# Kernel optimization log

Hardware: AMD Instinct MI355X
Metric: run time of the kernel (lower is better)

## Reference

```python
import jax, jax.numpy as jnp
import numpy as np

GROUPS = 32
EPS = 1e-5
NUM_HEADS = 8

def group_norm(x, w, b):
    # x: [B, C, H, W], normalize over (C//G, H, W) per group
    B, C, H, W = x.shape
    xg = x.reshape(B, GROUPS, C // GROUPS, H, W)
    mean = xg.mean(axis=(2, 3, 4), keepdims=True)
    var = xg.var(axis=(2, 3, 4), keepdims=True)
    xg = (xg - mean) * jax.lax.rsqrt(var + EPS)
    x = xg.reshape(B, C, H, W)
    return x * w[None, :, None, None] + b[None, :, None, None]

def setup_inputs() -> dict:
    key = jax.random.key(0)
    ks = jax.random.split(key, 3)
    C = 512
    x = jax.random.normal(ks[0], (8, C, 32, 32), dtype=jnp.float32)
    gn_w = jnp.ones((C,), jnp.float32)
    gn_b = jnp.zeros((C,), jnp.float32)
    # 1x1 conv weights stored as [out, in] matrices
    qkv_w = jax.random.normal(ks[1], (3 * C, C), dtype=jnp.float32) * (C ** -0.5)
    qkv_b = jnp.zeros((3 * C,), jnp.float32)
    proj_w = jax.random.normal(ks[2], (C, C), dtype=jnp.float32) * (C ** -0.5)
    proj_b = jnp.zeros((C,), jnp.float32)
    return {"x": x, "gn_w": gn_w, "gn_b": gn_b, "qkv_w": qkv_w,
            "qkv_b": qkv_b, "proj_w": proj_w, "proj_b": proj_b}

def reference(x, gn_w, gn_b, qkv_w, qkv_b, proj_w, proj_b):
    B, C, H, W = x.shape
    nh = NUM_HEADS
    hd = C // nh
    N = H * W
    residual = x
    xn = group_norm(x, gn_w, gn_b)
    # 1x1 conv == channel matmul: [B, 3C, H, W]
    qkv = jnp.einsum('bchw,oc->bohw', xn, qkv_w) + qkv_b[None, :, None, None]
    # [B, 3, nh, hd, N] -> q/k/v each [B, nh, N, hd]
    qkv = qkv.reshape(B, 3, nh, hd, N).transpose(1, 0, 2, 4, 3)
    q, k, v = qkv[0], qkv[1], qkv[2]
    scale = hd ** -0.5
    attn = jnp.einsum('bhqd,bhkd->bhqk', q, k) * scale
    attn = jax.nn.softmax(attn, axis=-1)
    out = jnp.einsum('bhqk,bhkd->bhqd', attn, v)  # [B, nh, N, hd]
    out = out.transpose(0, 1, 3, 2).reshape(B, C, H, W)
    out = jnp.einsum('bchw,oc->bohw', out, proj_w) + proj_b[None, :, None, None]
    return out + residual
```

## Files before the change

### kernel.cpp

```cpp
#include <hip/hip_runtime.h>


typedef __bf16 bf16;
typedef __bf16 bf16x8 __attribute__((ext_vector_type(8)));
typedef __bf16 bf16x4 __attribute__((ext_vector_type(4)));
typedef float  f32x4  __attribute__((ext_vector_type(4)));

#define MFMA_16x16x32(A, B, C) __builtin_amdgcn_mfma_f32_16x16x32_bf16((A), (B), (C), 0, 0, 0)

static __device__ __forceinline__ void async_stage_128x32(
    const bf16* __restrict__ g0, bf16* lds, int tid) {
  const int wv = tid >> 6, ln = tid & 63;
#pragma unroll
  for (int cc = 0; cc < 2; ++cc) {
    const int c = wv + cc * 4;
    const bf16* g = g0 + (size_t)(c * 16 + (ln >> 2)) * 512 + (ln & 3) * 8;
    __builtin_amdgcn_global_load_lds(
        (const __attribute__((address_space(1))) void*)g,
        (__attribute__((address_space(3))) void*)(lds + c * 512),
        16, 0, 0);
  }
}

__global__ void wconv_kernel(const float* __restrict__ qw, const float* __restrict__ pw,
                             bf16* __restrict__ wq, bf16* __restrict__ wp) {
  const int i = blockIdx.x * 256 + threadIdx.x;
  if (i < 1536 * 512) wq[i] = (bf16)qw[i];
  if (i < 512 * 512)  wp[i] = (bf16)pw[i];
}

__global__ void gn_stats_kernel(const float* __restrict__ x,
                                float* __restrict__ meanp, float* __restrict__ rstdp) {
  const int bg = blockIdx.x;
  const float4* p = (const float4*)(x + (size_t)bg * 16384);
  float s = 0.f, s2 = 0.f;
#pragma unroll 4
  for (int i = threadIdx.x; i < 4096; i += 256) {
    float4 v = p[i];
    s  += (v.x + v.y) + (v.z + v.w);
    s2 += (v.x * v.x + v.y * v.y) + (v.z * v.z + v.w * v.w);
  }
#pragma unroll
  for (int d = 1; d < 64; d <<= 1) {
    s  += __shfl_xor(s,  d);
    s2 += __shfl_xor(s2, d);
  }
  __shared__ float as[4], as2[4];
  if ((threadIdx.x & 63) == 0) { as[threadIdx.x >> 6] = s; as2[threadIdx.x >> 6] = s2; }
  __syncthreads();
  if (threadIdx.x == 0) {
    float S  = as[0] + as[1] + as[2] + as[3];
    float S2 = as2[0] + as2[1] + as2[2] + as2[3];
    float m = S * (1.0f / 16384.0f);
    float v = S2 * (1.0f / 16384.0f) - m * m;
    meanp[bg] = m;
    rstdp[bg] = rsqrtf(v + 1e-5f);
  }
}

__global__ void gn_apply_kernel(const float* __restrict__ x,
                                const float* __restrict__ gn_w, const float* __restrict__ gn_b,
                                const float* __restrict__ meanp, const float* __restrict__ rstdp,
                                bf16* __restrict__ xn_t) {
  const int n0 = blockIdx.x * 64, c0 = blockIdx.y * 64, b = blockIdx.z;
  __shared__ float tile[64 * 68];
  const int t = threadIdx.x;
  const float* xb = x + ((size_t)b * 512 + c0) * 1024 + n0;
#pragma unroll
  for (int i = 0; i < 4; ++i) {
    int idx = t + i * 256;
    int cl  = idx >> 4;
    int n4  = (idx & 15) * 4;
    float4 v = *(const float4*)(xb + (size_t)cl * 1024 + n4);
    int c  = c0 + cl;
    int bg = b * 32 + (c >> 4);
    float sc = rstdp[bg] * gn_w[c];
    float sh = gn_b[c] - meanp[bg] * sc;
    tile[(n4 + 0) * 68 + cl] = v.x * sc + sh;
    tile[(n4 + 1) * 68 + cl] = v.y * sc + sh;
    tile[(n4 + 2) * 68 + cl] = v.z * sc + sh;
    tile[(n4 + 3) * 68 + cl] = v.w * sc + sh;
  }
  __syncthreads();
  bf16* ob = xn_t + ((size_t)b * 1024 + n0) * 512 + c0;
#pragma unroll
  for (int i = 0; i < 16; ++i) {
    int idx = t + i * 256;
    int nl = idx >> 6, cl = idx & 63;
    ob[(size_t)nl * 512 + cl] = (bf16)tile[nl * 68 + cl];
  }
}

__global__ __launch_bounds__(256) void qkv_gemm_kernel(
    const bf16* __restrict__ W, const bf16* __restrict__ xn_t,
    const float* __restrict__ qkv_b, bf16* __restrict__ qkv_t,
    bf16* __restrict__ v_t) {
  const int n0 = blockIdx.x * 128;
  const int o0 = blockIdx.y * 128;
  const int b  = blockIdx.z;
  __shared__ bf16 As[2][128 * 32];
  __shared__ bf16 Bs[2][128 * 32];
  const int tid = threadIdx.x, ln = tid & 63, wv = tid >> 6;
  const int mw = (wv >> 1) * 64, nw = (wv & 1) * 64;
  const int l15 = ln & 15, lg = ln >> 4;
  const bf16* gA = W + (size_t)o0 * 512;
  const bf16* gB = xn_t + ((size_t)b * 1024 + n0) * 512;
  f32x4 acc[4][4] = {};
  for (int kk = 0; kk < 512; kk += 64) {
    async_stage_128x32(gA + kk,      As[0], tid);
    async_stage_128x32(gA + kk + 32, As[1], tid);
    async_stage_128x32(gB + kk,      Bs[0], tid);
    async_stage_128x32(gB + kk + 32, Bs[1], tid);
    __syncthreads();
#pragma unroll
    for (int p = 0; p < 2; ++p) {
      bf16x8 af[4], bfr[4];
#pragma unroll
      for (int mi = 0; mi < 4; ++mi)
        af[mi] = *(const bf16x8*)(&As[p][(mw + mi * 16 + l15) * 32 + lg * 8]);
#pragma unroll
      for (int nj = 0; nj < 4; ++nj)
        bfr[nj] = *(const bf16x8*)(&Bs[p][(nw + nj * 16 + l15) * 32 + lg * 8]);
#pragma unroll
      for (int mi = 0; mi < 4; ++mi)
#pragma unroll
        for (int nj = 0; nj < 4; ++nj)
          acc[mi][nj] = MFMA_16x16x32(af[mi], bfr[nj], acc[mi][nj]);
    }
    __syncthreads();
  }
  if (o0 < 1024) {
    const float qs = (o0 < 512) ? 0.125f * 1.44269504089f : 1.0f;
#pragma unroll
    for (int mi = 0; mi < 4; ++mi) {
      const int o = o0 + mw + mi * 16 + lg * 4;
      const float b0 = qkv_b[o], b1 = qkv_b[o + 1], b2 = qkv_b[o + 2], b3 = qkv_b[o + 3];
#pragma unroll
      for (int nj = 0; nj < 4; ++nj) {
        const int n = n0 + nw + nj * 16 + l15;
        f32x4 v = acc[mi][nj];
        bf16x4 st = { (bf16)((v.x + b0) * qs), (bf16)((v.y + b1) * qs),
                      (bf16)((v.z + b2) * qs), (bf16)((v.w + b3) * qs) };
        *(bf16x4*)(&qkv_t[((size_t)b * 1024 + n) * 1536 + o]) = st;
      }
    }
  } else {
#pragma unroll
    for (int mi = 0; mi < 4; ++mi) {
      const int o  = o0 + mw + mi * 16 + lg * 4;
      const int hd = o - 1024;
      const float b0 = qkv_b[o], b1 = qkv_b[o + 1], b2 = qkv_b[o + 2], b3 = qkv_b[o + 3];
      bf16* vb = v_t + ((size_t)b * 512 + hd) * 1024;
#pragma unroll
      for (int nj = 0; nj < 4; ++nj) {
        const int n = n0 + nw + nj * 16 + l15;
        f32x4 v = acc[mi][nj];
        vb[0 * 1024 + n] = (bf16)(v.x + b0);
        vb[1 * 1024 + n] = (bf16)(v.y + b1);
        vb[2 * 1024 + n] = (bf16)(v.z + b2);
        vb[3 * 1024 + n] = (bf16)(v.w + b3);
      }
    }
  }
}

__global__ __launch_bounds__(512, 4) void attn_kernel(
    const bf16* __restrict__ qkv_t, const bf16* __restrict__ v_t,
    bf16* __restrict__ at_t) {
  const int qt = blockIdx.x;
  const int b  = blockIdx.y >> 3;
  const int h  = blockIdx.y & 7;
  __shared__ __align__(16) char smem[73728];
  const int tid = threadIdx.x, ln = tid & 63, wv = tid >> 6;
  const int half = wv >> 2, w4 = wv & 3;
  const int l15 = ln & 15, g = ln >> 4;
  bf16* Kt = (bf16*)(smem + half * 18432);
  bf16* Vt = Kt + 64 * 72;
  bf16* Pme = (bf16*)(smem + 36864) + wv * 32 * 72;
  const bf16* hq  = qkv_t + (size_t)b * 1024 * 1536 + h * 64;
  const bf16* hk  = hq + 512;
  const bf16* vtb = v_t + (size_t)(b * 8 + h) * 64 * 1024;

  const int qb = qt * 128 + w4 * 32;
  bf16x8 qf[2][2];
#pragma unroll
  for (int m = 0; m < 2; ++m)
#pragma unroll
    for (int ks = 0; ks < 2; ++ks)
      qf[m][ks] = *(const bf16x8*)(hq + (size_t)(qb + m * 16 + l15) * 1536 + ks * 32 + g * 8);

  f32x4 oacc[2][4] = {};
  float lst[2] = { 0.f, 0.f };

  const int t256 = tid & 255;
  const int srow = t256 >> 2, scg = (t256 & 3) * 16;
  const int kt0 = half * 8;
  bf16x8 kpre0 = *(const bf16x8*)(hk + (size_t)(kt0 * 64 + srow) * 1536 + scg);
  bf16x8 kpre1 = *(const bf16x8*)(hk + (size_t)(kt0 * 64 + srow) * 1536 + scg + 8);
  bf16x8 vpre0 = *(const bf16x8*)(vtb + (size_t)srow * 1024 + kt0 * 64 + scg);
  bf16x8 vpre1 = *(const bf16x8*)(vtb + (size_t)srow * 1024 + kt0 * 64 + scg + 8);

  for (int i = 0; i < 8; ++i) {
    __syncthreads();
    *(bf16x8*)(&Kt[srow * 72 + scg])     = kpre0;
    *(bf16x8*)(&Kt[srow * 72 + scg + 8]) = kpre1;
    *(bf16x8*)(&Vt[srow * 72 + scg])     = vpre0;
    *(bf16x8*)(&Vt[srow * 72 + scg + 8]) = vpre1;
    __syncthreads();
    if (i < 7) {
      const int ktn = kt0 + i + 1;
      const bf16* hk2  = hk  + (size_t)(ktn * 64 + srow) * 1536 + scg;
      const bf16* vtb2 = vtb + (size_t)srow * 1024 + ktn * 64 + scg;
      kpre0 = *(const bf16x8*)(hk2);
      kpre1 = *(const bf16x8*)(hk2 + 8);
      vpre0 = *(const bf16x8*)(vtb2);
      vpre1 = *(const bf16x8*)(vtb2 + 8);
    }

    bf16x8 kf[4][2];
#pragma unroll
    for (int kj = 0; kj < 4; ++kj)
#pragma unroll
      for (int ks = 0; ks < 2; ++ks)
        kf[kj][ks] = *(const bf16x8*)(&Kt[(kj * 16 + l15) * 72 + ks * 32 + g * 8]);

#pragma unroll
    for (int m = 0; m < 2; ++m) {
      f32x4 st[4] = {};
#pragma unroll
      for (int ks = 0; ks < 2; ++ks)
#pragma unroll
        for (int kj = 0; kj < 4; ++kj)
          st[kj] = MFMA_16x16x32(kf[kj][ks], qf[m][ks], st[kj]);
      float rs = 0.f;
#pragma unroll
      for (int kj = 0; kj < 4; ++kj) {
        float e0 = exp2f(st[kj][0]);
        float e1 = exp2f(st[kj][1]);
        float e2 = exp2f(st[kj][2]);
        float e3 = exp2f(st[kj][3]);
        rs += (e0 + e1) + (e2 + e3);
        bf16x4 pe = { (bf16)e0, (bf16)e1, (bf16)e2, (bf16)e3 };
        *(bf16x4*)(&Pme[(m * 16 + l15) * 72 + kj * 16 + g * 4]) = pe;
      }
      lst[m] += rs;
    }

#pragma unroll
    for (int ks = 0; ks < 2; ++ks) {
      bf16x8 vf[4];
#pragma unroll
      for (int dt = 0; dt < 4; ++dt)
        vf[dt] = *(const bf16x8*)(&Vt[(dt * 16 + l15) * 72 + ks * 32 + g * 8]);
#pragma unroll
      for (int m = 0; m < 2; ++m) {
        bf16x8 pf = *(const bf16x8*)(&Pme[(m * 16 + l15) * 72 + ks * 32 + g * 8]);
#pragma unroll
        for (int dt = 0; dt < 4; ++dt)
          oacc[m][dt] = MFMA_16x16x32(vf[dt], pf, oacc[m][dt]);
      }
    }
  }

  float lfull[2];
#pragma unroll
  for (int m = 0; m < 2; ++m) {
    float l = lst[m];
    l += __shfl_xor(l, 16);
    l += __shfl_xor(l, 32);
    lfull[m] = l;
  }

  float* MB  = (float*)smem;
  float* MLb = (float*)(smem + 36864);
  __syncthreads();
  if (half == 1) {
    float* mb = MB + w4 * (32 * 68);
#pragma unroll
    for (int m = 0; m < 2; ++m) {
#pragma unroll
      for (int dt = 0; dt < 4; ++dt)
        *(f32x4*)(mb + (m * 16 + l15) * 68 + dt * 16 + g * 4) = oacc[m][dt];
      if (g == 0) MLb[w4 * 32 + (m * 16 + l15)] = lfull[m];
    }
  }
  __syncthreads();
  if (half == 0) {
    const float* mb = MB + w4 * (32 * 68);
#pragma unroll
    for (int m = 0; m < 2; ++m) {
      const float lB  = MLb[w4 * 32 + (m * 16 + l15)];
      const float inv = 1.0f / (lfull[m] + lB);
      const int q = qb + m * 16 + l15;
#pragma unroll
      for (int dt = 0; dt < 4; ++dt) {
        f32x4 ob = *(const f32x4*)(mb + (m * 16 + l15) * 68 + dt * 16 + g * 4);
        bf16x4 ov = { (bf16)((oacc[m][dt][0] + ob[0]) * inv),
                      (bf16)((oacc[m][dt][1] + ob[1]) * inv),
                      (bf16)((oacc[m][dt][2] + ob[2]) * inv),
                      (bf16)((oacc[m][dt][3] + ob[3]) * inv) };
        *(bf16x4*)(&at_t[((size_t)b * 1024 + q) * 512 + h * 64 + dt * 16 + g * 4]) = ov;
      }
    }
  }
}

__global__ __launch_bounds__(256) void proj_gemm_kernel(
    const bf16* __restrict__ at_t, const bf16* __restrict__ wp,
    const float* __restrict__ proj_b, const float* __restrict__ x,
    float* __restrict__ out) {
  const int i0 = blockIdx.x * 128;
  const int c0 = blockIdx.y * 128;
  const int b  = blockIdx.z;
  __shared__ bf16 As[2][128 * 32];
  __shared__ bf16 Bs[2][128 * 32];
  const int tid = threadIdx.x, ln = tid & 63, wv = tid >> 6;
  const int mw = (wv >> 1) * 64, nw = (wv & 1) * 64;
  const int l15 = ln & 15, lg = ln >> 4;
  const bf16* gA = at_t + ((size_t)b * 1024 + i0) * 512;
  const bf16* gB = wp + (size_t)c0 * 512;
  f32x4 acc[4][4] = {};
  for (int kk = 0; kk < 512; kk += 64) {
    async_stage_128x32(gA + kk,      As[0], tid);
    async_stage_128x32(gA + kk + 32, As[1], tid);
    async_stage_128x32(gB + kk,      Bs[0], tid);
    async_stage_128x32(gB + kk + 32, Bs[1], tid);
    __syncthreads();
#pragma unroll
    for (int p = 0; p < 2; ++p) {
      bf16x8 af[4], bfr[4];
#pragma unroll
      for (int mi = 0; mi < 4; ++mi)
        af[mi] = *(const bf16x8*)(&As[p][(mw + mi * 16 + l15) * 32 + lg * 8]);
#pragma unroll
      for (int nj = 0; nj < 4; ++nj)
        bfr[nj] = *(const bf16x8*)(&Bs[p][(nw + nj * 16 + l15) * 32 + lg * 8]);
#pragma unroll
      for (int mi = 0; mi < 4; ++mi)
#pragma unroll
        for (int nj = 0; nj < 4; ++nj)
          acc[mi][nj] = MFMA_16x16x32(af[mi], bfr[nj], acc[mi][nj]);
    }
    __syncthreads();
  }
#pragma unroll
  for (int mi = 0; mi < 4; ++mi) {
    const int i = i0 + mw + mi * 16 + lg * 4;
#pragma unroll
    for (int nj = 0; nj < 4; ++nj) {
      const int c = c0 + nw + nj * 16 + l15;
      const float bias = proj_b[c];
      const size_t off = ((size_t)b * 512 + c) * 1024 + i;
      const float4 res = *(const float4*)(x + off);
      f32x4 v = acc[mi][nj];
      float4 ov;
      ov.x = v.x + bias + res.x;
      ov.y = v.y + bias + res.y;
      ov.z = v.z + bias + res.z;
      ov.w = v.w + bias + res.w;
      *(float4*)(out + off) = ov;
    }
  }
}

extern "C" void kernel_launch(void* const* d_in, const int* in_sizes, int n_in,
                              void* d_out, int out_size, void* d_ws, size_t ws_size,
                              hipStream_t stream) {
  (void)in_sizes; (void)n_in; (void)out_size; (void)ws_size;
  const float* x      = (const float*)d_in[0];
  const float* gn_w   = (const float*)d_in[1];
  const float* gn_b   = (const float*)d_in[2];
  const float* qkv_w  = (const float*)d_in[3];
  const float* qkv_b  = (const float*)d_in[4];
  const float* proj_w = (const float*)d_in[5];
  const float* proj_b = (const float*)d_in[6];
  float* out = (float*)d_out;

  char* ws = (char*)d_ws;
  float* meanp = (float*)ws;
  float* rstdp = meanp + 256;
  bf16* wq    = (bf16*)(ws + 4096);
  bf16* wp    = wq + (size_t)1536 * 512;
  bf16* xn_t  = wp + (size_t)512 * 512;
  bf16* qkv_t = xn_t + (size_t)8 * 1024 * 512;
  bf16* at_t  = qkv_t + (size_t)8 * 1024 * 1536;
  bf16* v_t   = at_t + (size_t)8 * 1024 * 512;

  hipLaunchKernelGGL(wconv_kernel,    dim3(3072),      dim3(256), 0, stream, qkv_w, proj_w, wq, wp);
  hipLaunchKernelGGL(gn_stats_kernel, dim3(256),       dim3(256), 0, stream, x, meanp, rstdp);
  hipLaunchKernelGGL(gn_apply_kernel, dim3(16, 8, 8),  dim3(256), 0, stream, x, gn_w, gn_b, meanp, rstdp, xn_t);
  hipLaunchKernelGGL(qkv_gemm_kernel, dim3(8, 12, 8),  dim3(256), 0, stream, wq, xn_t, qkv_b, qkv_t, v_t);
  hipLaunchKernelGGL(attn_kernel,     dim3(8, 64),     dim3(512), 0, stream, qkv_t, v_t, at_t);
  hipLaunchKernelGGL(proj_gemm_kernel,dim3(8, 4, 8),   dim3(256), 0, stream, at_t, wp, proj_b, x, out);
}
```

Measured before the change: 165.0 us.

## Double-buffer GEMM K loops, merge prep kernels, halve proj GEMM tile

Both GEMMs now prefetch the next 32-wide K slice into the alternate LDS buffer while computing on the current one, with a single barrier per step, replacing the old load-all-then-compute pattern that had two barriers. The weight conversion and group-norm statistics kernels are merged into one launch, which removes a kernel launch. The projection GEMM uses 64-row tiles so its grid doubles to 512 blocks, giving better occupancy of the CUs. The trade-offs are more barrier iterations and a smaller MFMA tile per wave in the projection.

```diff
diff --git a/kernel.cpp b/kernel.cpp
--- a/kernel.cpp
+++ b/kernel.cpp
@@ -22,15 +22,26 @@
   }
 }
 
-__global__ void wconv_kernel(const float* __restrict__ qw, const float* __restrict__ pw,
-                             bf16* __restrict__ wq, bf16* __restrict__ wp) {
-  const int i = blockIdx.x * 256 + threadIdx.x;
-  if (i < 1536 * 512) wq[i] = (bf16)qw[i];
-  if (i < 512 * 512)  wp[i] = (bf16)pw[i];
-}
-
-__global__ void gn_stats_kernel(const float* __restrict__ x,
-                                float* __restrict__ meanp, float* __restrict__ rstdp) {
+static __device__ __forceinline__ void async_stage_64x32(
+    const bf16* __restrict__ g0, bf16* lds, int tid) {
+  const int wv = tid >> 6, ln = tid & 63;
+  const bf16* g = g0 + (size_t)(wv * 16 + (ln >> 2)) * 512 + (ln & 3) * 8;
+  __builtin_amdgcn_global_load_lds(
+      (const __attribute__((address_space(1))) void*)g,
+      (__attribute__((address_space(3))) void*)(lds + wv * 512),
+      16, 0, 0);
+}
+
+__global__ void prep_kernel(const float* __restrict__ x,
+                            float* __restrict__ meanp, float* __restrict__ rstdp,
+                            const float* __restrict__ qw, const float* __restrict__ pw,
+                            bf16* __restrict__ wq, bf16* __restrict__ wp) {
+  if (blockIdx.x >= 256) {
+    const int i = (blockIdx.x - 256) * 256 + threadIdx.x;
+    if (i < 1536 * 512) wq[i] = (bf16)qw[i];
+    if (i < 512 * 512)  wp[i] = (bf16)pw[i];
+    return;
+  }
   const int bg = blockIdx.x;
   const float4* p = (const float4*)(x + (size_t)bg * 16384);
   float s = 0.f, s2 = 0.f;
@@ -106,28 +117,27 @@
   const bf16* gA = W + (size_t)o0 * 512;
   const bf16* gB = xn_t + ((size_t)b * 1024 + n0) * 512;
   f32x4 acc[4][4] = {};
-  for (int kk = 0; kk < 512; kk += 64) {
-    async_stage_128x32(gA + kk,      As[0], tid);
-    async_stage_128x32(gA + kk + 32, As[1], tid);
-    async_stage_128x32(gB + kk,      Bs[0], tid);
-    async_stage_128x32(gB + kk + 32, Bs[1], tid);
+  async_stage_128x32(gA, As[0], tid);
+  async_stage_128x32(gB, Bs[0], tid);
+  for (int it = 0; it < 16; ++it) {
     __syncthreads();
-#pragma unroll
-    for (int p = 0; p < 2; ++p) {
-      bf16x8 af[4], bfr[4];
-#pragma unroll
-      for (int mi = 0; mi < 4; ++mi)
-        af[mi] = *(const bf16x8*)(&As[p][(mw + mi * 16 + l15) * 32 + lg * 8]);
+    const int cur = it & 1, nxt = cur ^ 1;
+    if (it < 15) {
+      async_stage_128x32(gA + (it + 1) * 32, As[nxt], tid);
+      async_stage_128x32(gB + (it + 1) * 32, Bs[nxt], tid);
+    }
+    bf16x8 af[4], bfr[4];
+#pragma unroll
+    for (int mi = 0; mi < 4; ++mi)
+      af[mi] = *(const bf16x8*)(&As[cur][(mw + mi * 16 + l15) * 32 + lg * 8]);
+#pragma unroll
+    for (int nj = 0; nj < 4; ++nj)
+      bfr[nj] = *(const bf16x8*)(&Bs[cur][(nw + nj * 16 + l15) * 32 + lg * 8]);
+#pragma unroll
+    for (int mi = 0; mi < 4; ++mi)
 #pragma unroll
       for (int nj = 0; nj < 4; ++nj)
-        bfr[nj] = *(const bf16x8*)(&Bs[p][(nw + nj * 16 + l15) * 32 + lg * 8]);
-#pragma unroll
-      for (int mi = 0; mi < 4; ++mi)
-#pragma unroll
-        for (int nj = 0; nj < 4; ++nj)
-          acc[mi][nj] = MFMA_16x16x32(af[mi], bfr[nj], acc[mi][nj]);
-    }
-    __syncthreads();
+        acc[mi][nj] = MFMA_16x16x32(af[mi], bfr[nj], acc[mi][nj]);
   }
   if (o0 < 1024) {
     const float qs = (o0 < 512) ? 0.125f * 1.44269504089f : 1.0f;
@@ -309,42 +319,41 @@
     const bf16* __restrict__ at_t, const bf16* __restrict__ wp,
     const float* __restrict__ proj_b, const float* __restrict__ x,
     float* __restrict__ out) {
-  const int i0 = blockIdx.x * 128;
+  const int i0 = blockIdx.x * 64;
   const int c0 = blockIdx.y * 128;
   const int b  = blockIdx.z;
-  __shared__ bf16 As[2][128 * 32];
+  __shared__ bf16 As[2][64 * 32];
   __shared__ bf16 Bs[2][128 * 32];
   const int tid = threadIdx.x, ln = tid & 63, wv = tid >> 6;
-  const int mw = (wv >> 1) * 64, nw = (wv & 1) * 64;
+  const int mw = (wv >> 1) * 32, nw = (wv & 1) * 64;
   const int l15 = ln & 15, lg = ln >> 4;
   const bf16* gA = at_t + ((size_t)b * 1024 + i0) * 512;
   const bf16* gB = wp + (size_t)c0 * 512;
-  f32x4 acc[4][4] = {};
-  for (int kk = 0; kk < 512; kk += 64) {
-    async_stage_128x32(gA + kk,      As[0], tid);
-    async_stage_128x32(gA + kk + 32, As[1], tid);
-    async_stage_128x32(gB + kk,      Bs[0], tid);
-    async_stage_128x32(gB + kk + 32, Bs[1], tid);
+  f32x4 acc[2][4] = {};
+  async_stage_64x32(gA, As[0], tid);
+  async_stage_128x32(gB, Bs[0], tid);
+  for (int it = 0; it < 16; ++it) {
     __syncthreads();
-#pragma unroll
-    for (int p = 0; p < 2; ++p) {
-      bf16x8 af[4], bfr[4];
-#pragma unroll
-      for (int mi = 0; mi < 4; ++mi)
-        af[mi] = *(const bf16x8*)(&As[p][(mw + mi * 16 + l15) * 32 + lg * 8]);
+    const int cur = it & 1, nxt = cur ^ 1;
+    if (it < 15) {
+      async_stage_64x32(gA + (it + 1) * 32, As[nxt], tid);
+      async_stage_128x32(gB + (it + 1) * 32, Bs[nxt], tid);
+    }
+    bf16x8 af[2], bfr[4];
+#pragma unroll
+    for (int mi = 0; mi < 2; ++mi)
+      af[mi] = *(const bf16x8*)(&As[cur][(mw + mi * 16 + l15) * 32 + lg * 8]);
+#pragma unroll
+    for (int nj = 0; nj < 4; ++nj)
+      bfr[nj] = *(const bf16x8*)(&Bs[cur][(nw + nj * 16 + l15) * 32 + lg * 8]);
+#pragma unroll
+    for (int mi = 0; mi < 2; ++mi)
 #pragma unroll
       for (int nj = 0; nj < 4; ++nj)
-        bfr[nj] = *(const bf16x8*)(&Bs[p][(nw + nj * 16 + l15) * 32 + lg * 8]);
-#pragma unroll
-      for (int mi = 0; mi < 4; ++mi)
-#pragma unroll
-        for (int nj = 0; nj < 4; ++nj)
-          acc[mi][nj] = MFMA_16x16x32(af[mi], bfr[nj], acc[mi][nj]);
-    }
-    __syncthreads();
-  }
-#pragma unroll
-  for (int mi = 0; mi < 4; ++mi) {
+        acc[mi][nj] = MFMA_16x16x32(af[mi], bfr[nj], acc[mi][nj]);
+  }
+#pragma unroll
+  for (int mi = 0; mi < 2; ++mi) {
     const int i = i0 + mw + mi * 16 + lg * 4;
 #pragma unroll
     for (int nj = 0; nj < 4; ++nj) {
@@ -386,10 +395,14 @@
   bf16* at_t  = qkv_t + (size_t)8 * 1024 * 1536;
   bf16* v_t   = at_t + (size_t)8 * 1024 * 512;
 
-  hipLaunchKernelGGL(wconv_kernel,    dim3(3072),      dim3(256), 0, stream, qkv_w, proj_w, wq, wp);
-  hipLaunchKernelGGL(gn_stats_kernel, dim3(256),       dim3(256), 0, stream, x, meanp, rstdp);
-  hipLaunchKernelGGL(gn_apply_kernel, dim3(16, 8, 8),  dim3(256), 0, stream, x, gn_w, gn_b, meanp, rstdp, xn_t);
-  hipLaunchKernelGGL(qkv_gemm_kernel, dim3(8, 12, 8),  dim3(256), 0, stream, wq, xn_t, qkv_b, qkv_t, v_t);
-  hipLaunchKernelGGL(attn_kernel,     dim3(8, 64),     dim3(512), 0, stream, qkv_t, v_t, at_t);
-  hipLaunchKernelGGL(proj_gemm_kernel,dim3(8, 4, 8),   dim3(256), 0, stream, at_t, wp, proj_b, x, out);
-}
+  hipLaunchKernelGGL(prep_kernel,     dim3(3328),      dim3(256), 0, stream,
+                     x, meanp, rstdp, qkv_w, proj_w, wq, wp);
+  hipLaunchKernelGGL(gn_apply_kernel, dim3(16, 8, 8),  dim3(256), 0, stream,
+                     x, gn_w, gn_b, meanp, rstdp, xn_t);
+  hipLaunchKernelGGL(qkv_gemm_kernel, dim3(8, 12, 8),  dim3(256), 0, stream,
+                     wq, xn_t, qkv_b, qkv_t, v_t);
+  hipLaunchKernelGGL(attn_kernel,     dim3(8, 64),     dim3(512), 0, stream,
+                     qkv_t, v_t, at_t);
+  hipLaunchKernelGGL(proj_gemm_kernel,dim3(16, 4, 8),  dim3(256), 0, stream,
+                     at_t, wp, proj_b, x, out);
+}
```

Result: faster. 161.2 us (-2.3%).
